# Performance work log

Hardware: AMD Instinct MI355X
Metric: run time of the kernel (lower is better)

## Reference

```python
import jax, jax.numpy as jnp
import numpy as np
import math

NUM_HEADS = 16

def setup_inputs() -> dict:
    key = jax.random.key(0)
    ks = jax.random.split(key, 5)
    d_model = 1024
    std = math.sqrt(2.0 / (d_model + d_model))
    x = jax.random.normal(ks[0], (2, 2048, d_model), dtype=jnp.float32)
    Wq = jax.random.normal(ks[1], (d_model, d_model), dtype=jnp.float32) * std
    Wk = jax.random.normal(ks[2], (d_model, d_model), dtype=jnp.float32) * std
    Wv = jax.random.normal(ks[3], (d_model, d_model), dtype=jnp.float32) * std
    Wo = jax.random.normal(ks[4], (d_model, d_model), dtype=jnp.float32) * std
    return {"x": x, "Wq": Wq, "Wk": Wk, "Wv": Wv, "Wo": Wo}

def reference(x, Wq, Wk, Wv, Wo):
    # x: [b, s, d]; W*: [d_out, d_in]
    b, s, d = x.shape
    h = NUM_HEADS
    dh = d // h
    def proj(W):
        y = jnp.einsum('bsd,ed->bse', x, W)           # [b, s, d]
        return y.reshape(b, s, h, dh).transpose(0, 2, 1, 3)  # [b, h, s, dh]
    Q, K, V = proj(Wq), proj(Wk), proj(Wv)
    scale = 1.0 / math.sqrt(dh)
    logits = jnp.einsum('bhqd,bhkd->bhqk', Q, K) * scale  # [b, h, s, s]
    causal = jnp.tril(jnp.ones((s, s), dtype=bool))
    logits = jnp.where(causal, logits, -jnp.inf)
    attn = jax.nn.softmax(logits, axis=-1)
    out = jnp.einsum('bhqk,bhkd->bhqd', attn, V)          # [b, h, s, dh]
    out = out.transpose(0, 2, 1, 3).reshape(b, s, d)
    return jnp.einsum('bsv,dv->bsd', out, Wo)
```

## Files before the change

### kernel.cpp

```cpp
#include <hip/hip_runtime.h>
#include <hip/hip_bf16.h>
#include <math.h>

typedef unsigned short ushort_t;
typedef __attribute__((ext_vector_type(8))) short bf16x8;
typedef __attribute__((ext_vector_type(4))) float f32x4;

#define MFMA16(a,b,c) __builtin_amdgcn_mfma_f32_16x16x32_bf16(a,b,c,0,0,0)
#define QSCALE 0.1803368801111204f

typedef unsigned int u32;
typedef __attribute__((address_space(1))) const u32* gp1_t;
typedef __attribute__((address_space(3))) u32* lp3_t;

__device__ __forceinline__ void async_copy16(void* l, const void* g) {
    __builtin_amdgcn_global_load_lds((gp1_t)g, (lp3_t)l, 16, 0, 0);
}

__device__ __forceinline__ ushort_t f2bf(float f) {
    unsigned u = __float_as_uint(f);
    unsigned r = u + 0x7fffu + ((u >> 16) & 1u);
    return (ushort_t)(r >> 16);
}

__global__ __launch_bounds__(256) void cvt_kernel(
    const float* __restrict__ x,  const float* __restrict__ wq,
    const float* __restrict__ wk, const float* __restrict__ wv,
    const float* __restrict__ wo, ushort_t* __restrict__ dst)
{
    size_t base = ((size_t)blockIdx.x * 256 + threadIdx.x) * 8;
    const float* src; size_t off;
    if      (base < 4194304ul) { src = x;  off = base; }
    else if (base < 5242880ul) { src = wq; off = base - 4194304ul; }
    else if (base < 6291456ul) { src = wk; off = base - 5242880ul; }
    else if (base < 7340032ul) { src = wv; off = base - 6291456ul; }
    else                       { src = wo; off = base - 7340032ul; }
    float4 a = *(const float4*)(src + off);
    float4 b = *(const float4*)(src + off + 4);
    struct alignas(16) U8 { ushort_t v[8]; } o;
    o.v[0]=f2bf(a.x); o.v[1]=f2bf(a.y); o.v[2]=f2bf(a.z); o.v[3]=f2bf(a.w);
    o.v[4]=f2bf(b.x); o.v[5]=f2bf(b.y); o.v[6]=f2bf(b.z); o.v[7]=f2bf(b.w);
    *(U8*)(dst + base) = o;
}

__global__ __launch_bounds__(256) void gemm_bt(
    const ushort_t* __restrict__ A, const ushort_t* __restrict__ B,
    ushort_t* __restrict__ Oq, ushort_t* __restrict__ Ok,
    ushort_t* __restrict__ Ovt, float* __restrict__ Of, int is_out)
{
    __shared__ ushort_t As[2][128 * 64];
    __shared__ ushort_t Bs[2][128 * 64];
    const int t = threadIdx.x, l = t & 63, w = t >> 6;
    const int l4 = l >> 4, lm = l & 15;
    const int wr = w >> 1, wc = w & 1;

    const int nwg = gridDim.x * gridDim.y;
    const int orig = (int)blockIdx.y * gridDim.x + (int)blockIdx.x;
    const int qq = nwg >> 3;
    const int swz = (orig & 7) * qq + (orig >> 3);
    const int n0 = (swz % gridDim.x) * 128;
    const int m0 = (swz / gridDim.x) * 128;

    const int srow = t >> 3, scol = t & 7;

    f32x4 acc[4][4] = {};

    #pragma unroll
    for (int i = 0; i < 4; ++i) {
        const int row = i * 32 + srow;
        const int c = scol ^ (row & 7);
        async_copy16((char*)&As[0][0] + i * 4096 + t * 16,
                     A + (size_t)(m0 + row) * 1024 + c * 8);
        async_copy16((char*)&Bs[0][0] + i * 4096 + t * 16,
                     B + (size_t)(n0 + row) * 1024 + c * 8);
    }

    for (int kt = 0; kt < 16; ++kt) {
        const int cur = kt & 1;
        if (kt + 1 < 16) {
            const int k0 = (kt + 1) * 64;
            #pragma unroll
            for (int i = 0; i < 4; ++i) {
                const int row = i * 32 + srow;
                const int c = scol ^ (row & 7);
                async_copy16((char*)&As[cur ^ 1][0] + i * 4096 + t * 16,
                             A + (size_t)(m0 + row) * 1024 + k0 + c * 8);
                async_copy16((char*)&Bs[cur ^ 1][0] + i * 4096 + t * 16,
                             B + (size_t)(n0 + row) * 1024 + k0 + c * 8);
            }
            asm volatile("s_waitcnt vmcnt(8)" ::: "memory");
        } else {
            asm volatile("s_waitcnt vmcnt(0)" ::: "memory");
        }
        __builtin_amdgcn_s_barrier();

        #pragma unroll
        for (int ks = 0; ks < 2; ++ks) {
            bf16x8 af[4], bfr[4];
            #pragma unroll
            for (int mi = 0; mi < 4; ++mi) {
                const int row = wr * 64 + mi * 16 + lm;
                const int ch = l4 + 4 * ks;
                af[mi] = *(const bf16x8*)(&As[cur][0] + row * 64 + ((ch ^ (row & 7)) << 3));
            }
            #pragma unroll
            for (int ni = 0; ni < 4; ++ni) {
                const int row = wc * 64 + ni * 16 + lm;
                const int ch = l4 + 4 * ks;
                bfr[ni] = *(const bf16x8*)(&Bs[cur][0] + row * 64 + ((ch ^ (row & 7)) << 3));
            }
            #pragma unroll
            for (int mi = 0; mi < 4; ++mi)
                #pragma unroll
                for (int ni = 0; ni < 4; ++ni)
                    acc[mi][ni] = MFMA16(af[mi], bfr[ni], acc[mi][ni]);
        }
        asm volatile("s_waitcnt lgkmcnt(0)" ::: "memory");
        __builtin_amdgcn_s_barrier();
    }

    const int mb = m0 + wr * 64, nb = n0 + wc * 64;
    if (is_out) {
        #pragma unroll
        for (int mi = 0; mi < 4; ++mi)
            #pragma unroll
            for (int ni = 0; ni < 4; ++ni) {
                const int n = nb + ni * 16 + lm;
                const int mr = mb + mi * 16 + l4 * 4;
                #pragma unroll
                for (int r = 0; r < 4; ++r)
                    Of[(size_t)(mr + r) * 1024 + n] = acc[mi][ni][r];
            }
    } else if (nb >= 2048) {
        #pragma unroll
        for (int mi = 0; mi < 4; ++mi)
            #pragma unroll
            for (int ni = 0; ni < 4; ++ni) {
                const int nv = nb - 2048 + ni * 16 + lm;
                const int m = mb + mi * 16 + l4 * 4;
                const int b = m >> 11, s = m & 2047, h = nv >> 6, d = nv & 63;
                ushort4 pk;
                pk.x = f2bf(acc[mi][ni][0]); pk.y = f2bf(acc[mi][ni][1]);
                pk.z = f2bf(acc[mi][ni][2]); pk.w = f2bf(acc[mi][ni][3]);
                *(ushort4*)(Ovt + (((size_t)(b * 16 + h) * 64 + d) * 2048 + s)) = pk;
            }
    } else {
        ushort_t* O = (nb < 1024) ? Oq : Ok;
        const float qs = (nb < 1024) ? (float)QSCALE : 1.0f;
        const int nbase = nb & 1023;
        #pragma unroll
        for (int mi = 0; mi < 4; ++mi)
            #pragma unroll
            for (int ni = 0; ni < 4; ++ni) {
                const int n = nbase + ni * 16 + lm;
                const int h = n >> 6, d = n & 63;
                #pragma unroll
                for (int r = 0; r < 4; ++r) {
                    const int m = mb + mi * 16 + l4 * 4 + r;
                    const int b = m >> 11, s = m & 2047;
                    O[((size_t)(b * 16 + h) * 2048 + s) * 64 + d] =
                        f2bf(acc[mi][ni][r] * qs);
                }
            }
    }
}

template<bool MASK>
__device__ __forceinline__ void attn_tile(
    const ushort_t* Kbuf, const ushort_t* Vbuf, ushort_t* Pw,
    const bf16x8 (&qf)[2], const bf16x8 ones,
    f32x4 (&o)[4], f32x4& ol, float& m_run,
    int kv0, int qrow, int l4, int lm)
{
    f32x4 sf[4] = {};
    #pragma unroll
    for (int ks = 0; ks < 2; ++ks)
        #pragma unroll
        for (int cf = 0; cf < 4; ++cf) {
            const int rowK = cf * 16 + lm;
            const int ch = l4 + 4 * ks;
            bf16x8 kf = *(const bf16x8*)(Kbuf + rowK * 64 + ((ch ^ (rowK & 7)) << 3));
            sf[cf] = MFMA16(kf, qf[ks], sf[cf]);
        }

    float tmax = -1e30f;
    #pragma unroll
    for (int cf = 0; cf < 4; ++cf)
        #pragma unroll
        for (int r = 0; r < 4; ++r) {
            float v = sf[cf][r];
            if (MASK && (kv0 + cf * 16 + l4 * 4 + r > qrow)) v = -30000.f;
            sf[cf][r] = v;
            tmax = fmaxf(tmax, v);
        }
    tmax = fmaxf(tmax, __shfl_xor(tmax, 16));
    tmax = fmaxf(tmax, __shfl_xor(tmax, 32));

    if (!__all(tmax <= m_run + 8.f)) {
        const float mn = fmaxf(m_run, tmax);
        const float alpha = __builtin_amdgcn_exp2f(m_run - mn);
        #pragma unroll
        for (int df = 0; df < 4; ++df)
            #pragma unroll
            for (int r = 0; r < 4; ++r)
                o[df][r] *= alpha;
        #pragma unroll
        for (int r = 0; r < 4; ++r) ol[r] *= alpha;
        m_run = mn;
    }

    #pragma unroll
    for (int cf = 0; cf < 4; ++cf) {
        float p0 = __builtin_amdgcn_exp2f(sf[cf][0] - m_run);
        float p1 = __builtin_amdgcn_exp2f(sf[cf][1] - m_run);
        float p2 = __builtin_amdgcn_exp2f(sf[cf][2] - m_run);
        float p3 = __builtin_amdgcn_exp2f(sf[cf][3] - m_run);
        __hip_bfloat162 b01 = __float22bfloat162_rn(make_float2(p0, p1));
        __hip_bfloat162 b23 = __float22bfloat162_rn(make_float2(p2, p3));
        uint2 pkv;
        __builtin_memcpy(&pkv.x, &b01, 4);
        __builtin_memcpy(&pkv.y, &b23, 4);
        *(uint2*)&Pw[lm * 72 + cf * 16 + l4 * 4] = pkv;
    }

    #pragma unroll
    for (int ks = 0; ks < 2; ++ks) {
        bf16x8 pf = *(const bf16x8*)&Pw[lm * 72 + ks * 32 + l4 * 8];
        #pragma unroll
        for (int df = 0; df < 4; ++df) {
            const int rowV = df * 16 + lm;
            const int ch = l4 + 4 * ks;
            bf16x8 vf = *(const bf16x8*)(Vbuf + rowV * 64 + ((ch ^ (rowV & 7)) << 3));
            o[df] = MFMA16(vf, pf, o[df]);
        }
        ol = MFMA16(ones, pf, ol);
    }
}

__global__ __launch_bounds__(256) void attn_kernel(
    const ushort_t* __restrict__ Qg, const ushort_t* __restrict__ Kg,
    const ushort_t* __restrict__ Vtg, ushort_t* __restrict__ Og)
{
    __shared__ ushort_t Ks[2][64 * 64];
    __shared__ ushort_t Vs[2][64 * 64];
    __shared__ ushort_t Ps[4][16 * 72];
    const int t = threadIdx.x, l = t & 63, w = t >> 6;
    const int l4 = l >> 4, lm = l & 15;
    const int bh = blockIdx.x;
    const int qt = 31 - (int)blockIdx.y;
    const int q0 = qt * 64, q0w = q0 + w * 16;
    const int qrow = q0w + lm;

    bf16x8 qf[2];
    {
        const ushort_t* qp = Qg + ((size_t)bh * 2048 + qrow) * 64 + l4 * 8;
        qf[0] = *(const bf16x8*)qp;
        qf[1] = *(const bf16x8*)(qp + 32);
    }
    bf16x8 ones;
    #pragma unroll
    for (int i = 0; i < 8; ++i) ones[i] = (short)0x3F80;

    f32x4 o[4] = {};
    f32x4 ol = {};
    float m_run = -1e30f;

    const int nkv = qt + 1, last = nkv - 1;
    const int srow = t >> 3, scol = t & 7;
    const ushort_t* kg0 = Kg + ((size_t)bh * 2048 + srow) * 64 + (scol ^ (srow & 7)) * 8;
    const ushort_t* vg0 = Vtg + ((size_t)bh * 64 + srow) * 2048 + (scol ^ (srow & 7)) * 8;

    async_copy16((char*)&Ks[0][0] + t * 16, kg0);
    async_copy16((char*)&Vs[0][0] + t * 16, vg0);
    async_copy16((char*)&Ks[0][0] + 4096 + t * 16, kg0 + 32 * 64);
    async_copy16((char*)&Vs[0][0] + 4096 + t * 16, vg0 + 32 * 2048);
    __syncthreads();

    for (int kt = 0; kt < last; ++kt) {
        const int cur = kt & 1;
        const size_t koff = (size_t)(kt + 1) * 64 * 64;
        const size_t voff = (size_t)(kt + 1) * 64;
        async_copy16((char*)&Ks[cur ^ 1][0] + t * 16, kg0 + koff);
        async_copy16((char*)&Vs[cur ^ 1][0] + t * 16, vg0 + voff);
        async_copy16((char*)&Ks[cur ^ 1][0] + 4096 + t * 16, kg0 + koff + 32 * 64);
        async_copy16((char*)&Vs[cur ^ 1][0] + 4096 + t * 16, vg0 + voff + 32 * 2048);

        attn_tile<false>(&Ks[cur][0], &Vs[cur][0], &Ps[w][0],
                         qf, ones, o, ol, m_run, kt * 64, qrow, l4, lm);
        __syncthreads();
    }
    attn_tile<true>(&Ks[last & 1][0], &Vs[last & 1][0], &Ps[w][0],
                    qf, ones, o, ol, m_run, last * 64, qrow, l4, lm);

    const int b = bh >> 4, h = bh & 15;
    const float inv = 1.f / ol[0];
    #pragma unroll
    for (int df = 0; df < 4; ++df) {
        ushort4 pk4;
        pk4.x = f2bf(o[df][0] * inv); pk4.y = f2bf(o[df][1] * inv);
        pk4.z = f2bf(o[df][2] * inv); pk4.w = f2bf(o[df][3] * inv);
        *(ushort4*)&Og[((size_t)(b * 2048 + qrow)) * 1024 + h * 64 + df * 16 + l4 * 4] = pk4;
    }
}

extern "C" void kernel_launch(void* const* d_in, const int* in_sizes, int n_in,
                              void* d_out, int out_size, void* d_ws, size_t ws_size,
                              hipStream_t stream)
{
    const float* x  = (const float*)d_in[0];
    const float* Wq = (const float*)d_in[1];
    const float* Wk = (const float*)d_in[2];
    const float* Wv = (const float*)d_in[3];
    const float* Wo = (const float*)d_in[4];

    ushort_t* ws  = (ushort_t*)d_ws;
    ushort_t* xb  = ws;
    ushort_t* wqb = ws + 4194304;
    ushort_t* wob = ws + 7340032;
    ushort_t* Qw  = ws + 8388608;
    ushort_t* Kw  = ws + 12582912;
    ushort_t* Vtw = ws + 16777216;
    ushort_t* Aow = ws + 20971520;

    cvt_kernel<<<4096, 256, 0, stream>>>(x, Wq, Wk, Wv, Wo, ws);
    gemm_bt<<<dim3(24, 32), 256, 0, stream>>>(xb, wqb, Qw, Kw, Vtw, nullptr, 0);
    attn_kernel<<<dim3(32, 32), 256, 0, stream>>>(Qw, Kw, Vtw, Aow);
    gemm_bt<<<dim3(8, 32), 256, 0, stream>>>(Aow, wob, nullptr, nullptr, nullptr,
                                             (float*)d_out, 1);
}
```

Before: 117.6 us.

## Widen GEMM blocks to 512 threads and double attention query tile per wave

The projection GEMMs now run 8 waves of 512 threads per 128x128 tile, each wave owning a 32x64 sub-tile, which halves per-thread accumulators and loads. The attention kernel gives each wave 32 query rows (two 16-row fragments) instead of 16, so each K/V fragment read from LDS feeds two MFMAs and the query tile grows to 128 rows per block, halving grid size. The causal diagonal now spans two masked KV tiles, handled with a second masked loop. The trade-off is higher register pressure in attention and fewer blocks for load balance.

```diff
diff --git a/kernel.cpp b/kernel.cpp
--- a/kernel.cpp
+++ b/kernel.cpp
@@ -43,7 +43,7 @@
     *(U8*)(dst + base) = o;
 }
 
-__global__ __launch_bounds__(256) void gemm_bt(
+__global__ __launch_bounds__(512) void gemm_bt(
     const ushort_t* __restrict__ A, const ushort_t* __restrict__ B,
     ushort_t* __restrict__ Oq, ushort_t* __restrict__ Ok,
     ushort_t* __restrict__ Ovt, float* __restrict__ Of, int is_out)
@@ -63,15 +63,15 @@
 
     const int srow = t >> 3, scol = t & 7;
 
-    f32x4 acc[4][4] = {};
-
-    #pragma unroll
-    for (int i = 0; i < 4; ++i) {
-        const int row = i * 32 + srow;
+    f32x4 acc[2][4] = {};
+
+    #pragma unroll
+    for (int i = 0; i < 2; ++i) {
+        const int row = i * 64 + srow;
         const int c = scol ^ (row & 7);
-        async_copy16((char*)&As[0][0] + i * 4096 + t * 16,
+        async_copy16((char*)&As[0][0] + i * 8192 + t * 16,
                      A + (size_t)(m0 + row) * 1024 + c * 8);
-        async_copy16((char*)&Bs[0][0] + i * 4096 + t * 16,
+        async_copy16((char*)&Bs[0][0] + i * 8192 + t * 16,
                      B + (size_t)(n0 + row) * 1024 + c * 8);
     }
 
@@ -80,15 +80,15 @@
         if (kt + 1 < 16) {
             const int k0 = (kt + 1) * 64;
             #pragma unroll
-            for (int i = 0; i < 4; ++i) {
-                const int row = i * 32 + srow;
+            for (int i = 0; i < 2; ++i) {
+                const int row = i * 64 + srow;
                 const int c = scol ^ (row & 7);
-                async_copy16((char*)&As[cur ^ 1][0] + i * 4096 + t * 16,
+                async_copy16((char*)&As[cur ^ 1][0] + i * 8192 + t * 16,
                              A + (size_t)(m0 + row) * 1024 + k0 + c * 8);
-                async_copy16((char*)&Bs[cur ^ 1][0] + i * 4096 + t * 16,
+                async_copy16((char*)&Bs[cur ^ 1][0] + i * 8192 + t * 16,
                              B + (size_t)(n0 + row) * 1024 + k0 + c * 8);
             }
-            asm volatile("s_waitcnt vmcnt(8)" ::: "memory");
+            asm volatile("s_waitcnt vmcnt(4)" ::: "memory");
         } else {
             asm volatile("s_waitcnt vmcnt(0)" ::: "memory");
         }
@@ -96,10 +96,10 @@
 
         #pragma unroll
         for (int ks = 0; ks < 2; ++ks) {
-            bf16x8 af[4], bfr[4];
-            #pragma unroll
-            for (int mi = 0; mi < 4; ++mi) {
-                const int row = wr * 64 + mi * 16 + lm;
+            bf16x8 af[2], bfr[4];
+            #pragma unroll
+            for (int mi = 0; mi < 2; ++mi) {
+                const int row = wr * 32 + mi * 16 + lm;
                 const int ch = l4 + 4 * ks;
                 af[mi] = *(const bf16x8*)(&As[cur][0] + row * 64 + ((ch ^ (row & 7)) << 3));
             }
@@ -110,7 +110,7 @@
                 bfr[ni] = *(const bf16x8*)(&Bs[cur][0] + row * 64 + ((ch ^ (row & 7)) << 3));
             }
             #pragma unroll
-            for (int mi = 0; mi < 4; ++mi)
+            for (int mi = 0; mi < 2; ++mi)
                 #pragma unroll
                 for (int ni = 0; ni < 4; ++ni)
                     acc[mi][ni] = MFMA16(af[mi], bfr[ni], acc[mi][ni]);
@@ -119,10 +119,10 @@
         __builtin_amdgcn_s_barrier();
     }
 
-    const int mb = m0 + wr * 64, nb = n0 + wc * 64;
+    const int mb = m0 + wr * 32, nb = n0 + wc * 64;
     if (is_out) {
         #pragma unroll
-        for (int mi = 0; mi < 4; ++mi)
+        for (int mi = 0; mi < 2; ++mi)
             #pragma unroll
             for (int ni = 0; ni < 4; ++ni) {
                 const int n = nb + ni * 16 + lm;
@@ -133,7 +133,7 @@
             }
     } else if (nb >= 2048) {
         #pragma unroll
-        for (int mi = 0; mi < 4; ++mi)
+        for (int mi = 0; mi < 2; ++mi)
             #pragma unroll
             for (int ni = 0; ni < 4; ++ni) {
                 const int nv = nb - 2048 + ni * 16 + lm;
@@ -149,7 +149,7 @@
         const float qs = (nb < 1024) ? (float)QSCALE : 1.0f;
         const int nbase = nb & 1023;
         #pragma unroll
-        for (int mi = 0; mi < 4; ++mi)
+        for (int mi = 0; mi < 2; ++mi)
             #pragma unroll
             for (int ni = 0; ni < 4; ++ni) {
                 const int n = nbase + ni * 16 + lm;
@@ -168,11 +168,11 @@
 template<bool MASK>
 __device__ __forceinline__ void attn_tile(
     const ushort_t* Kbuf, const ushort_t* Vbuf, ushort_t* Pw,
-    const bf16x8 (&qf)[2], const bf16x8 ones,
-    f32x4 (&o)[4], f32x4& ol, float& m_run,
-    int kv0, int qrow, int l4, int lm)
-{
-    f32x4 sf[4] = {};
+    const bf16x8 (&qf)[2][2], const bf16x8 ones,
+    f32x4 (&o)[2][4], f32x4 (&ol)[2], float (&m_run)[2],
+    int kv0, int q0w, int l4, int lm)
+{
+    f32x4 sf[2][4] = {};
     #pragma unroll
     for (int ks = 0; ks < 2; ++ks)
         #pragma unroll
@@ -180,60 +180,73 @@
             const int rowK = cf * 16 + lm;
             const int ch = l4 + 4 * ks;
             bf16x8 kf = *(const bf16x8*)(Kbuf + rowK * 64 + ((ch ^ (rowK & 7)) << 3));
-            sf[cf] = MFMA16(kf, qf[ks], sf[cf]);
-        }
-
-    float tmax = -1e30f;
-    #pragma unroll
-    for (int cf = 0; cf < 4; ++cf)
-        #pragma unroll
-        for (int r = 0; r < 4; ++r) {
-            float v = sf[cf][r];
-            if (MASK && (kv0 + cf * 16 + l4 * 4 + r > qrow)) v = -30000.f;
-            sf[cf][r] = v;
-            tmax = fmaxf(tmax, v);
-        }
-    tmax = fmaxf(tmax, __shfl_xor(tmax, 16));
-    tmax = fmaxf(tmax, __shfl_xor(tmax, 32));
-
-    if (!__all(tmax <= m_run + 8.f)) {
-        const float mn = fmaxf(m_run, tmax);
-        const float alpha = __builtin_amdgcn_exp2f(m_run - mn);
-        #pragma unroll
-        for (int df = 0; df < 4; ++df)
-            #pragma unroll
-            for (int r = 0; r < 4; ++r)
-                o[df][r] *= alpha;
-        #pragma unroll
-        for (int r = 0; r < 4; ++r) ol[r] *= alpha;
-        m_run = mn;
-    }
-
-    #pragma unroll
-    for (int cf = 0; cf < 4; ++cf) {
-        float p0 = __builtin_amdgcn_exp2f(sf[cf][0] - m_run);
-        float p1 = __builtin_amdgcn_exp2f(sf[cf][1] - m_run);
-        float p2 = __builtin_amdgcn_exp2f(sf[cf][2] - m_run);
-        float p3 = __builtin_amdgcn_exp2f(sf[cf][3] - m_run);
-        __hip_bfloat162 b01 = __float22bfloat162_rn(make_float2(p0, p1));
-        __hip_bfloat162 b23 = __float22bfloat162_rn(make_float2(p2, p3));
-        uint2 pkv;
-        __builtin_memcpy(&pkv.x, &b01, 4);
-        __builtin_memcpy(&pkv.y, &b23, 4);
-        *(uint2*)&Pw[lm * 72 + cf * 16 + l4 * 4] = pkv;
-    }
+            sf[0][cf] = MFMA16(kf, qf[0][ks], sf[0][cf]);
+            sf[1][cf] = MFMA16(kf, qf[1][ks], sf[1][cf]);
+        }
+
+    float tmax[2] = {-1e30f, -1e30f};
+    #pragma unroll
+    for (int qi = 0; qi < 2; ++qi) {
+        const int qrow = q0w + qi * 16 + lm;
+        #pragma unroll
+        for (int cf = 0; cf < 4; ++cf)
+            #pragma unroll
+            for (int r = 0; r < 4; ++r) {
+                float v = sf[qi][cf][r];
+                if (MASK && (kv0 + cf * 16 + l4 * 4 + r > qrow)) v = -30000.f;
+                sf[qi][cf][r] = v;
+                tmax[qi] = fmaxf(tmax[qi], v);
+            }
+        tmax[qi] = fmaxf(tmax[qi], __shfl_xor(tmax[qi], 16));
+        tmax[qi] = fmaxf(tmax[qi], __shfl_xor(tmax[qi], 32));
+    }
+
+    if (!__all(fmaxf(tmax[0] - m_run[0], tmax[1] - m_run[1]) <= 8.f)) {
+        #pragma unroll
+        for (int qi = 0; qi < 2; ++qi) {
+            const float mn = fmaxf(m_run[qi], tmax[qi]);
+            const float alpha = __builtin_amdgcn_exp2f(m_run[qi] - mn);
+            #pragma unroll
+            for (int df = 0; df < 4; ++df)
+                #pragma unroll
+                for (int r = 0; r < 4; ++r)
+                    o[qi][df][r] *= alpha;
+            #pragma unroll
+            for (int r = 0; r < 4; ++r) ol[qi][r] *= alpha;
+            m_run[qi] = mn;
+        }
+    }
+
+    #pragma unroll
+    for (int qi = 0; qi < 2; ++qi)
+        #pragma unroll
+        for (int cf = 0; cf < 4; ++cf) {
+            float p0 = __builtin_amdgcn_exp2f(sf[qi][cf][0] - m_run[qi]);
+            float p1 = __builtin_amdgcn_exp2f(sf[qi][cf][1] - m_run[qi]);
+            float p2 = __builtin_amdgcn_exp2f(sf[qi][cf][2] - m_run[qi]);
+            float p3 = __builtin_amdgcn_exp2f(sf[qi][cf][3] - m_run[qi]);
+            __hip_bfloat162 b01 = __float22bfloat162_rn(make_float2(p0, p1));
+            __hip_bfloat162 b23 = __float22bfloat162_rn(make_float2(p2, p3));
+            uint2 pkv;
+            __builtin_memcpy(&pkv.x, &b01, 4);
+            __builtin_memcpy(&pkv.y, &b23, 4);
+            *(uint2*)&Pw[(qi * 16 + lm) * 72 + cf * 16 + l4 * 4] = pkv;
+        }
 
     #pragma unroll
     for (int ks = 0; ks < 2; ++ks) {
-        bf16x8 pf = *(const bf16x8*)&Pw[lm * 72 + ks * 32 + l4 * 8];
+        bf16x8 pf0 = *(const bf16x8*)&Pw[(0 * 16 + lm) * 72 + ks * 32 + l4 * 8];
+        bf16x8 pf1 = *(const bf16x8*)&Pw[(1 * 16 + lm) * 72 + ks * 32 + l4 * 8];
         #pragma unroll
         for (int df = 0; df < 4; ++df) {
             const int rowV = df * 16 + lm;
             const int ch = l4 + 4 * ks;
             bf16x8 vf = *(const bf16x8*)(Vbuf + rowV * 64 + ((ch ^ (rowV & 7)) << 3));
-            o[df] = MFMA16(vf, pf, o[df]);
-        }
-        ol = MFMA16(ones, pf, ol);
+            o[0][df] = MFMA16(vf, pf0, o[0][df]);
+            o[1][df] = MFMA16(vf, pf1, o[1][df]);
+        }
+        ol[0] = MFMA16(ones, pf0, ol[0]);
+        ol[1] = MFMA16(ones, pf1, ol[1]);
     }
 }
 
@@ -243,29 +256,29 @@
 {
     __shared__ ushort_t Ks[2][64 * 64];
     __shared__ ushort_t Vs[2][64 * 64];
-    __shared__ ushort_t Ps[4][16 * 72];
+    __shared__ ushort_t Ps[4][32 * 72];
     const int t = threadIdx.x, l = t & 63, w = t >> 6;
     const int l4 = l >> 4, lm = l & 15;
     const int bh = blockIdx.x;
-    const int qt = 31 - (int)blockIdx.y;
-    const int q0 = qt * 64, q0w = q0 + w * 16;
-    const int qrow = q0w + lm;
-
-    bf16x8 qf[2];
-    {
-        const ushort_t* qp = Qg + ((size_t)bh * 2048 + qrow) * 64 + l4 * 8;
-        qf[0] = *(const bf16x8*)qp;
-        qf[1] = *(const bf16x8*)(qp + 32);
+    const int qt = 15 - (int)blockIdx.y;
+    const int q0 = qt * 128, q0w = q0 + w * 32;
+
+    bf16x8 qf[2][2];
+    #pragma unroll
+    for (int qi = 0; qi < 2; ++qi) {
+        const ushort_t* qp = Qg + ((size_t)bh * 2048 + q0w + qi * 16 + lm) * 64 + l4 * 8;
+        qf[qi][0] = *(const bf16x8*)qp;
+        qf[qi][1] = *(const bf16x8*)(qp + 32);
     }
     bf16x8 ones;
     #pragma unroll
     for (int i = 0; i < 8; ++i) ones[i] = (short)0x3F80;
 
-    f32x4 o[4] = {};
-    f32x4 ol = {};
-    float m_run = -1e30f;
-
-    const int nkv = qt + 1, last = nkv - 1;
+    f32x4 o[2][4] = {};
+    f32x4 ol[2] = {};
+    float m_run[2] = {-1e30f, -1e30f};
+
+    const int nkv = 2 * qt + 2;
     const int srow = t >> 3, scol = t & 7;
     const ushort_t* kg0 = Kg + ((size_t)bh * 2048 + srow) * 64 + (scol ^ (srow & 7)) * 8;
     const ushort_t* vg0 = Vtg + ((size_t)bh * 64 + srow) * 2048 + (scol ^ (srow & 7)) * 8;
@@ -276,7 +289,8 @@
     async_copy16((char*)&Vs[0][0] + 4096 + t * 16, vg0 + 32 * 2048);
     __syncthreads();
 
-    for (int kt = 0; kt < last; ++kt) {
+    int kt = 0;
+    for (; kt < nkv - 2; ++kt) {
         const int cur = kt & 1;
         const size_t koff = (size_t)(kt + 1) * 64 * 64;
         const size_t voff = (size_t)(kt + 1) * 64;
@@ -286,20 +300,36 @@
         async_copy16((char*)&Vs[cur ^ 1][0] + 4096 + t * 16, vg0 + voff + 32 * 2048);
 
         attn_tile<false>(&Ks[cur][0], &Vs[cur][0], &Ps[w][0],
-                         qf, ones, o, ol, m_run, kt * 64, qrow, l4, lm);
+                         qf, ones, o, ol, m_run, kt * 64, q0w, l4, lm);
         __syncthreads();
     }
-    attn_tile<true>(&Ks[last & 1][0], &Vs[last & 1][0], &Ps[w][0],
-                    qf, ones, o, ol, m_run, last * 64, qrow, l4, lm);
+    for (; kt < nkv; ++kt) {
+        const int cur = kt & 1;
+        if (kt + 1 < nkv) {
+            const size_t koff = (size_t)(kt + 1) * 64 * 64;
+            const size_t voff = (size_t)(kt + 1) * 64;
+            async_copy16((char*)&Ks[cur ^ 1][0] + t * 16, kg0 + koff);
+            async_copy16((char*)&Vs[cur ^ 1][0] + t * 16, vg0 + voff);
+            async_copy16((char*)&Ks[cur ^ 1][0] + 4096 + t * 16, kg0 + koff + 32 * 64);
+            async_copy16((char*)&Vs[cur ^ 1][0] + 4096 + t * 16, vg0 + voff + 32 * 2048);
+        }
+        attn_tile<true>(&Ks[cur][0], &Vs[cur][0], &Ps[w][0],
+                        qf, ones, o, ol, m_run, kt * 64, q0w, l4, lm);
+        __syncthreads();
+    }
 
     const int b = bh >> 4, h = bh & 15;
-    const float inv = 1.f / ol[0];
-    #pragma unroll
-    for (int df = 0; df < 4; ++df) {
-        ushort4 pk4;
-        pk4.x = f2bf(o[df][0] * inv); pk4.y = f2bf(o[df][1] * inv);
-        pk4.z = f2bf(o[df][2] * inv); pk4.w = f2bf(o[df][3] * inv);
-        *(ushort4*)&Og[((size_t)(b * 2048 + qrow)) * 1024 + h * 64 + df * 16 + l4 * 4] = pk4;
+    #pragma unroll
+    for (int qi = 0; qi < 2; ++qi) {
+        const float inv = 1.f / ol[qi][0];
+        const int srow_o = q0w + qi * 16 + lm;
+        #pragma unroll
+        for (int df = 0; df < 4; ++df) {
+            ushort4 pk4;
+            pk4.x = f2bf(o[qi][df][0] * inv); pk4.y = f2bf(o[qi][df][1] * inv);
+            pk4.z = f2bf(o[qi][df][2] * inv); pk4.w = f2bf(o[qi][df][3] * inv);
+            *(ushort4*)&Og[((size_t)(b * 2048 + srow_o)) * 1024 + h * 64 + df * 16 + l4 * 4] = pk4;
+        }
     }
 }
 
@@ -323,8 +353,8 @@
     ushort_t* Aow = ws + 20971520;
 
     cvt_kernel<<<4096, 256, 0, stream>>>(x, Wq, Wk, Wv, Wo, ws);
-    gemm_bt<<<dim3(24, 32), 256, 0, stream>>>(xb, wqb, Qw, Kw, Vtw, nullptr, 0);
-    attn_kernel<<<dim3(32, 32), 256, 0, stream>>>(Qw, Kw, Vtw, Aow);
-    gemm_bt<<<dim3(8, 32), 256, 0, stream>>>(Aow, wob, nullptr, nullptr, nullptr,
+    gemm_bt<<<dim3(24, 32), 512, 0, stream>>>(xb, wqb, Qw, Kw, Vtw, nullptr, 0);
+    attn_kernel<<<dim3(32, 16), 256, 0, stream>>>(Qw, Kw, Vtw, Aow);
+    gemm_bt<<<dim3(8, 32), 512, 0, stream>>>(Aow, wob, nullptr, nullptr, nullptr,
                                              (float*)d_out, 1);
 }
```

Measured after the change: 117.4 us. No clear change (-0.2%).
